# Kernel optimization log

Hardware: AMD Instinct MI355X
Metric: run time of the kernel (lower is better)

The kernel has to match this reference:

```python
import jax, jax.numpy as jnp
import numpy as np

B, S, D = 2, 2048, 2048
H = 16
HD = D // H  # 128

def setup_inputs() -> dict:
    key = jax.random.key(0)
    k1, k2, k3 = jax.random.split(key, 3)
    x = jax.random.normal(k1, (B, S, D), dtype=jnp.float32)
    w_qkv = jax.random.normal(k2, (D, 3 * D), dtype=jnp.float32) * (1.0 / np.sqrt(D))
    b_qkv = jnp.zeros((3 * D,), dtype=jnp.float32)
    w_out = jax.random.normal(k3, (D, D), dtype=jnp.float32) * (1.0 / np.sqrt(D))
    b_out = jnp.zeros((D,), dtype=jnp.float32)
    return {"x": x, "w_qkv": w_qkv, "b_qkv": b_qkv, "w_out": w_out, "b_out": b_out}

def reference(x, w_qkv, b_qkv, w_out, b_out):
    batch, seq_len, channels = x.shape
    qkv = x @ w_qkv + b_qkv                      # [B,S,3D]
    q, k, v = jnp.split(qkv, 3, axis=-1)
    # [B,S,D] -> [B,H,S,HD]
    def heads(t):
        return t.reshape(batch, seq_len, H, HD).transpose(0, 2, 1, 3)
    q, k, v = heads(q), heads(k), heads(v)
    scale = 1.0 / np.sqrt(HD).astype(np.float32)
    attn = jnp.einsum('bhqd,bhkd->bhqk', q, k) * scale
    causal = jnp.tril(jnp.ones((seq_len, seq_len), dtype=bool))
    attn = jnp.where(causal, attn, -jnp.inf)
    attn = jax.nn.softmax(attn, axis=-1)
    y = jnp.einsum('bhqk,bhkd->bhqd', attn, v)   # [B,H,S,HD]
    y = y.transpose(0, 2, 1, 3).reshape(batch, seq_len, channels)
    return y @ w_out + b_out
```

## Files before the change

kernel.cpp:

```cpp
#include <hip/hip_runtime.h>
#include <hip/hip_bf16.h>
#include <cstdint>
#include <cstddef>

#define BB 2
#define SS 2048
#define DD 2048
#define HH 16
#define HDIM 128
#define QSCALE 0.12751743f

typedef short bf16x8 __attribute__((ext_vector_type(8)));
typedef float f32x4 __attribute__((ext_vector_type(4)));
typedef float f32x16 __attribute__((ext_vector_type(16)));

__device__ __forceinline__ ushort f2bf(float f) {
    union { float f; uint32_t u; } v; v.f = f;
    uint32_t u = v.u;
    u += 0x7fffu + ((u >> 16) & 1u);
    return (ushort)(u >> 16);
}

__device__ __forceinline__ ushort f2bf_fast(float f) {
    union { float f; uint32_t u; } v; v.f = f;
    return (ushort)((v.u + 0x8000u) >> 16);
}

__device__ __forceinline__ void gl16(const ushort* g, ushort* l) {
    __builtin_amdgcn_global_load_lds(
        (const __attribute__((address_space(1))) unsigned int*)g,
        (__attribute__((address_space(3))) unsigned int*)l,
        16, 0, 0);
}


__global__ __launch_bounds__(256) void cast_x_kernel(
    const float* __restrict__ X, ushort* __restrict__ Xb)
{
    size_t idx = ((size_t)blockIdx.x * 256 + threadIdx.x) * 8;
    float4 a = *(const float4*)(X + idx);
    float4 b = *(const float4*)(X + idx + 4);
    ushort4 o0, o1;
    o0.x = f2bf(a.x); o0.y = f2bf(a.y); o0.z = f2bf(a.z); o0.w = f2bf(a.w);
    o1.x = f2bf(b.x); o1.y = f2bf(b.y); o1.z = f2bf(b.z); o1.w = f2bf(b.w);
    *(ushort4*)(Xb + idx) = o0;
    *(ushort4*)(Xb + idx + 4) = o1;
}

__global__ __launch_bounds__(256) void transpose_cast_kernel(
    const float* __restrict__ W, ushort* __restrict__ Wt, int K, int N)
{
    __shared__ ushort tile[32][36];
    const int n0 = blockIdx.x * 32;
    const int k0 = blockIdx.y * 32;
    const int t = threadIdx.x;
    const int r = t >> 3;
    const int c = (t & 7) * 4;
    float4 a = *(const float4*)(W + (size_t)(k0 + r) * N + n0 + c);
    tile[r][c + 0] = f2bf(a.x); tile[r][c + 1] = f2bf(a.y);
    tile[r][c + 2] = f2bf(a.z); tile[r][c + 3] = f2bf(a.w);
    __syncthreads();
    ushort4 o;
    o.x = tile[c + 0][r]; o.y = tile[c + 1][r];
    o.z = tile[c + 2][r]; o.w = tile[c + 3][r];
    *(ushort4*)(Wt + (size_t)(n0 + r) * K + k0 + c) = o;
}

__global__ __launch_bounds__(256) void transpose_v_kernel(
    const ushort* __restrict__ V, ushort* __restrict__ Vt)
{
    __shared__ ushort tile[32][36];
    const int s0 = blockIdx.x * 32;
    const int h0 = blockIdx.y * 32;
    const int bh = blockIdx.z;
    const ushort* Vp = V + (size_t)bh * SS * HDIM;
    ushort* Vtp = Vt + (size_t)bh * HDIM * SS;
    const int t = threadIdx.x;
    const int r = t >> 3;
    const int c = (t & 7) * 4;
    *(ushort4*)&tile[r][c] = *(const ushort4*)(Vp + (size_t)(s0 + r) * HDIM + h0 + c);
    __syncthreads();
    ushort4 o;
    o.x = tile[c + 0][r]; o.y = tile[c + 1][r];
    o.z = tile[c + 2][r]; o.w = tile[c + 3][r];
    *(ushort4*)(Vtp + (size_t)(h0 + r) * SS + s0 + c) = o;
}

__global__ __launch_bounds__(256) void gemm_qkv_kernel(
    const ushort* __restrict__ A, const ushort* __restrict__ Bt,
    const float* __restrict__ bias,
    ushort* __restrict__ Qo, ushort* __restrict__ Ko, ushort* __restrict__ Vo)
{
    const int n0 = blockIdx.x * 128;
    const int m0 = blockIdx.y * 128;
    __shared__ ushort As[128 * 32];
    __shared__ ushort Bs[128 * 32];
    const int t = threadIdx.x, w = t >> 6, lane = t & 63;
    const int l31 = lane & 31, hh = lane >> 5;
    const int lrow = lane >> 2, lks = lane & 3;
    const int wr = w >> 1, wc = w & 1;
    const int swst = (lrow >> 1) & 3;
    const int swr  = (l31 >> 1) & 3;

    f32x16 acc[2][2];
#pragma unroll
    for (int i = 0; i < 2; ++i)
#pragma unroll
        for (int j = 0; j < 2; ++j) acc[i][j] = (f32x16)0.f;

    for (int k0 = 0; k0 < DD; k0 += 32) {
        __syncthreads();
#pragma unroll
        for (int q = 0; q < 2; ++q) {
            int e = w * 2 + q;
            int row = e * 16 + lrow;
            gl16(A  + (size_t)(m0 + row) * DD + k0 + (lks ^ swst) * 8, &As[e * 512]);
            gl16(Bt + (size_t)(n0 + row) * DD + k0 + (lks ^ swst) * 8, &Bs[e * 512]);
        }
        __syncthreads();
#pragma unroll
        for (int k16 = 0; k16 < 2; ++k16) {
            int co = ((k16 * 2 + hh) ^ swr) * 8;
            bf16x8 ar0 = *(const bf16x8*)&As[(wr * 64 + l31) * 32 + co];
            bf16x8 ar1 = *(const bf16x8*)&As[(wr * 64 + 32 + l31) * 32 + co];
            bf16x8 br0 = *(const bf16x8*)&Bs[(wc * 64 + l31) * 32 + co];
            bf16x8 br1 = *(const bf16x8*)&Bs[(wc * 64 + 32 + l31) * 32 + co];
            acc[0][0] = __builtin_amdgcn_mfma_f32_32x32x16_bf16(ar0, br0, acc[0][0], 0, 0, 0);
            acc[0][1] = __builtin_amdgcn_mfma_f32_32x32x16_bf16(ar0, br1, acc[0][1], 0, 0, 0);
            acc[1][0] = __builtin_amdgcn_mfma_f32_32x32x16_bf16(ar1, br0, acc[1][0], 0, 0, 0);
            acc[1][1] = __builtin_amdgcn_mfma_f32_32x32x16_bf16(ar1, br1, acc[1][1], 0, 0, 0);
        }
    }

    const int bidx = m0 >> 11;
    const int which = n0 >> 11;
    ushort* dst = (which == 0) ? Qo : ((which == 1) ? Ko : Vo);
    const float sc = (which == 0) ? QSCALE : 1.0f;
#pragma unroll
    for (int j = 0; j < 2; ++j) {
        int n = n0 + wc * 64 + j * 32 + l31;
        int c = n & 2047, h = c >> 7, hd = c & 127;
        float bv = bias[n];
        size_t base = ((size_t)(bidx * HH + h) * SS) * HDIM + hd;
#pragma unroll
        for (int i = 0; i < 2; ++i) {
#pragma unroll
            for (int r = 0; r < 16; ++r) {
                int s = (m0 & 2047) + wr * 64 + i * 32 + (r & 3) + 8 * (r >> 2) + 4 * hh;
                dst[base + (size_t)s * HDIM] = f2bf((acc[i][j][r] + bv) * sc);
            }
        }
    }
}

__global__ __launch_bounds__(256) void gemm_out_kernel(
    const ushort* __restrict__ A, const ushort* __restrict__ Bt,
    const float* __restrict__ bias, float* __restrict__ Out)
{
    const int n0 = blockIdx.x * 128;
    const int m0 = blockIdx.y * 128;
    __shared__ ushort As[128 * 32];
    __shared__ ushort Bs[128 * 32];
    const int t = threadIdx.x, w = t >> 6, lane = t & 63;
    const int l31 = lane & 31, hh = lane >> 5;
    const int lrow = lane >> 2, lks = lane & 3;
    const int wr = w >> 1, wc = w & 1;
    const int swst = (lrow >> 1) & 3;
    const int swr  = (l31 >> 1) & 3;

    f32x16 acc[2][2];
#pragma unroll
    for (int i = 0; i < 2; ++i)
#pragma unroll
        for (int j = 0; j < 2; ++j) acc[i][j] = (f32x16)0.f;

    for (int k0 = 0; k0 < DD; k0 += 32) {
        __syncthreads();
#pragma unroll
        for (int q = 0; q < 2; ++q) {
            int e = w * 2 + q;
            int row = e * 16 + lrow;
            gl16(A  + (size_t)(m0 + row) * DD + k0 + (lks ^ swst) * 8, &As[e * 512]);
            gl16(Bt + (size_t)(n0 + row) * DD + k0 + (lks ^ swst) * 8, &Bs[e * 512]);
        }
        __syncthreads();
#pragma unroll
        for (int k16 = 0; k16 < 2; ++k16) {
            int co = ((k16 * 2 + hh) ^ swr) * 8;
            bf16x8 ar0 = *(const bf16x8*)&As[(wr * 64 + l31) * 32 + co];
            bf16x8 ar1 = *(const bf16x8*)&As[(wr * 64 + 32 + l31) * 32 + co];
            bf16x8 br0 = *(const bf16x8*)&Bs[(wc * 64 + l31) * 32 + co];
            bf16x8 br1 = *(const bf16x8*)&Bs[(wc * 64 + 32 + l31) * 32 + co];
            acc[0][0] = __builtin_amdgcn_mfma_f32_32x32x16_bf16(ar0, br0, acc[0][0], 0, 0, 0);
            acc[0][1] = __builtin_amdgcn_mfma_f32_32x32x16_bf16(ar0, br1, acc[0][1], 0, 0, 0);
            acc[1][0] = __builtin_amdgcn_mfma_f32_32x32x16_bf16(ar1, br0, acc[1][0], 0, 0, 0);
            acc[1][1] = __builtin_amdgcn_mfma_f32_32x32x16_bf16(ar1, br1, acc[1][1], 0, 0, 0);
        }
    }

#pragma unroll
    for (int j = 0; j < 2; ++j) {
        int n = n0 + wc * 64 + j * 32 + l31;
        float bv = bias[n];
#pragma unroll
        for (int i = 0; i < 2; ++i) {
#pragma unroll
            for (int r = 0; r < 16; ++r) {
                int m = m0 + wr * 64 + i * 32 + (r & 3) + 8 * (r >> 2) + 4 * hh;
                Out[(size_t)m * DD + n] = acc[i][j][r] + bv;
            }
        }
    }
}

__global__ __launch_bounds__(256, 2) void attn_mfma_kernel(
    const ushort* __restrict__ Q, const ushort* __restrict__ K,
    const ushort* __restrict__ Vt, ushort* __restrict__ Y)
{
    const int bh = blockIdx.y;
    const int qt = gridDim.x - 1 - blockIdx.x;
    const int q0 = qt * 128;
    const int b = bh >> 4, h = bh & 15;

    __shared__ ushort Ks[4 * 64 * 32];
    __shared__ ushort Vs[2 * 128 * 32];
    __shared__ ushort Ps[128 * 32];

    const int t = threadIdx.x, w = t >> 6, lane = t & 63;
    const int l31 = lane & 31, hh = lane >> 5;
    const int lrow = lane >> 2, lks = lane & 3;
    const int swst = (lrow >> 1) & 3;
    const int swr  = (l31 >> 1) & 3;

    const ushort* Qp = Q  + (size_t)bh * SS * HDIM;
    const ushort* Kp = K  + (size_t)bh * SS * HDIM;
    const ushort* Vp = Vt + (size_t)bh * HDIM * SS;

    bf16x8 aq[8];
#pragma unroll
    for (int kb2 = 0; kb2 < 8; ++kb2)
        aq[kb2] = *(const bf16x8*)(Qp + (size_t)(q0 + w * 32 + l31) * HDIM + kb2 * 16 + hh * 8);

    bf16x8 ones;
#pragma unroll
    for (int j = 0; j < 8; ++j) ones[j] = (short)0x3F80;

    f32x16 O[4];
#pragma unroll
    for (int nt = 0; nt < 4; ++nt) O[nt] = (f32x16)0.f;
    f32x16 Ol = (f32x16)0.f;

    const int kbdiag = 2 * qt + (w >> 1);
    const int nkb = 2 * qt + 2;

    for (int kb = 0; kb < nkb; ++kb) {
        const int kbase = kb * 64;
        __syncthreads();
#pragma unroll
        for (int g = 0; g < 4; ++g) {
            int key = g * 16 + lrow;
            gl16(Kp + (size_t)(kbase + key) * HDIM + w * 32 + (lks ^ swst) * 8,
                 &Ks[w * 2048 + g * 512]);
        }
#pragma unroll
        for (int g = 0; g < 4; ++g) {
            int pan = g >> 1, sub = g & 1;
            int dim = w * 32 + sub * 16 + lrow;
            gl16(Vp + (size_t)dim * SS + kbase + pan * 32 + (lks ^ swst) * 8,
                 &Vs[pan * 4096 + (w * 32 + sub * 16) * 32]);
        }
        __syncthreads();

        const bool active = (kb <= kbdiag);
        if (active) {
            f32x16 sc0 = (f32x16)0.f, sc1 = (f32x16)0.f;
#pragma unroll
            for (int kb2 = 0; kb2 < 8; ++kb2) {
                int co = (((kb2 & 1) * 2 + hh) ^ swr) * 8;
                bf16x8 bk0 = *(const bf16x8*)&Ks[(kb2 >> 1) * 2048 + l31 * 32 + co];
                bf16x8 bk1 = *(const bf16x8*)&Ks[(kb2 >> 1) * 2048 + (32 + l31) * 32 + co];
                sc0 = __builtin_amdgcn_mfma_f32_32x32x16_bf16(aq[kb2], bk0, sc0, 0, 0, 0);
                sc1 = __builtin_amdgcn_mfma_f32_32x32x16_bf16(aq[kb2], bk1, sc1, 0, 0, 0);
            }

            if (kb == kbdiag) {
#pragma unroll
                for (int r = 0; r < 16; ++r) {
                    int rowg = q0 + w * 32 + (r & 3) + 8 * (r >> 2) + 4 * hh;
                    if (kbase + l31 > rowg)      sc0[r] = -1e30f;
                    if (kbase + 32 + l31 > rowg) sc1[r] = -1e30f;
                }
            }

#pragma unroll
            for (int half = 0; half < 2; ++half) {
#pragma unroll
                for (int r = 0; r < 16; ++r) {
                    float sv = (half == 0) ? sc0[r] : sc1[r];
                    float p = __builtin_amdgcn_exp2f(sv);
                    int rowm = (r & 3) + 8 * (r >> 2) + 4 * hh;
                    int pc = (l31 >> 3) ^ ((rowm >> 1) & 3);
                    Ps[(w * 32 + rowm) * 32 + (pc << 3) + (l31 & 7)] = f2bf_fast(p);
                }
#pragma unroll
                for (int kblk2 = 0; kblk2 < 2; ++kblk2) {
                    int co = ((kblk2 * 2 + hh) ^ swr) * 8;
                    bf16x8 ap = *(const bf16x8*)&Ps[(w * 32 + l31) * 32 + co];
#pragma unroll
                    for (int nt = 0; nt < 4; ++nt) {
                        bf16x8 bv = *(const bf16x8*)&Vs[half * 4096 + (nt * 32 + l31) * 32 + co];
                        O[nt] = __builtin_amdgcn_mfma_f32_32x32x16_bf16(ap, bv, O[nt], 0, 0, 0);
                    }
                    Ol = __builtin_amdgcn_mfma_f32_32x32x16_bf16(ap, ones, Ol, 0, 0, 0);
                }
            }
        }
    }

#pragma unroll
    for (int r = 0; r < 16; ++r) {
        int s = q0 + w * 32 + (r & 3) + 8 * (r >> 2) + 4 * hh;
        float inv = 1.0f / Ol[r];
        size_t base = ((size_t)(b * SS + s)) * DD + h * HDIM;
#pragma unroll
        for (int nt = 0; nt < 4; ++nt)
            Y[base + nt * 32 + l31] = f2bf(O[nt][r] * inv);
    }
}

extern "C" void kernel_launch(void* const* d_in, const int* in_sizes, int n_in,
                              void* d_out, int out_size, void* d_ws, size_t ws_size,
                              hipStream_t stream) {
    const float* x     = (const float*)d_in[0];
    const float* w_qkv = (const float*)d_in[1];
    const float* b_qkv = (const float*)d_in[2];
    const float* w_out = (const float*)d_in[3];
    const float* b_out = (const float*)d_in[4];
    float* out = (float*)d_out;

    ushort* ws  = (ushort*)d_ws;
    ushort* xb  = ws;
    ushort* wtq = xb + 8388608;
    ushort* wto = wtq + 12582912;
    ushort* q   = wto + 4194304;
    ushort* k   = q + 8388608;
    ushort* v   = k + 8388608;
    ushort* vt  = v + 8388608;
    ushort* y   = vt + 8388608;

    cast_x_kernel<<<4096, 256, 0, stream>>>(x, xb);
    transpose_cast_kernel<<<dim3(192, 64), 256, 0, stream>>>(w_qkv, wtq, DD, 3 * DD);
    transpose_cast_kernel<<<dim3(64, 64), 256, 0, stream>>>(w_out, wto, DD, DD);
    gemm_qkv_kernel<<<dim3(48, 32), 256, 0, stream>>>(xb, wtq, b_qkv, q, k, v);
    transpose_v_kernel<<<dim3(64, 4, 32), 256, 0, stream>>>(v, vt);
    attn_mfma_kernel<<<dim3(16, 32), 256, 0, stream>>>(q, k, vt, y);
    gemm_out_kernel<<<dim3(16, 32), 256, 0, stream>>>(y, wto, b_out, out);
}
```

Baseline: 408.0 us.

## Rewrite QKV GEMM with 256x256 tiles, double-buffered LDS and ping-pong scheduling

Replaces the 128x128 single-buffered QKV projection GEMM with a 512-thread, 256x256-tile kernel. It uses a BK=64 double-buffered LDS pipeline, staggered global_load_lds prefetches interleaved with 16x16x32 MFMA phases, s_setprio, and an XCD-aware block remapping. The goal is to raise data reuse and hide global-load latency behind MFMA work, cutting memory-bound stalls in the largest GEMM. In exchange it uses much more LDS (128KB) and many more accumulator registers, so occupancy drops to one block per CU and correctness depends on hand-placed waitcnts.

```diff
diff --git a/kernel.cpp b/kernel.cpp
--- a/kernel.cpp
+++ b/kernel.cpp
@@ -32,7 +32,6 @@
         (__attribute__((address_space(3))) unsigned int*)l,
         16, 0, 0);
 }
-
 
 __global__ __launch_bounds__(256) void cast_x_kernel(
     const float* __restrict__ X, ushort* __restrict__ Xb)
@@ -86,10 +85,174 @@
     *(ushort4*)(Vtp + (size_t)(h0 + r) * SS + s0 + c) = o;
 }
 
-__global__ __launch_bounds__(256) void gemm_qkv_kernel(
+#define NTK 32
+
+__global__ __launch_bounds__(512) void gemm_qkv_kernel(
     const ushort* __restrict__ A, const ushort* __restrict__ Bt,
     const float* __restrict__ bias,
     ushort* __restrict__ Qo, ushort* __restrict__ Ko, ushort* __restrict__ Vo)
+{
+    const int bid = blockIdx.x;
+    const int wgid = (bid & 7) * 48 + (bid >> 3);
+    const int mt = wgid / 24;
+    const int nt = wgid - mt * 24;
+    const int m0 = mt * 256, n0 = nt * 256;
+
+    __shared__ ushort As[2][2][8192];
+    __shared__ ushort Bs[2][2][8192];
+
+    const int tid = threadIdx.x;
+    const int w = tid >> 6, lane = tid & 63;
+    const int wr = w >> 2, wc = w & 3;
+    const int l15 = lane & 15, l4x = lane >> 4, l7 = lane & 7;
+
+    const int rt  = w * 8 + (lane >> 3);
+    const int giA = (lane & 7) ^ (lane >> 3);
+    const size_t aoff = (size_t)(m0 + rt) * DD + giA * 8;
+    const int nb = (w >> 2) * 64 + (w & 3) * 8 + (lane >> 3);
+    const size_t boff = (size_t)(n0 + nb) * DD + giA * 8;
+    const int ldst = w * 512;
+
+    const int rdA = (wr * 64 + l15) << 7;
+    const int rdB = (wc * 32 + l15) << 7;
+    const int cb0 = (l4x ^ l7) << 4;
+    const int cb1 = ((l4x ^ l7) ^ 4) << 4;
+
+#define STAGE_A(t, qm) do { \
+    gl16(A + aoff + (size_t)((qm) * 64) * DD + (t) * 64,       &As[(t) & 1][qm][ldst]); \
+    gl16(A + aoff + (size_t)(128 + (qm) * 64) * DD + (t) * 64, &As[(t) & 1][qm][4096 + ldst]); \
+} while (0)
+#define STAGE_B(t, qn) do { \
+    gl16(Bt + boff + (size_t)((qn) * 32) * DD + (t) * 64,       &Bs[(t) & 1][qn][ldst]); \
+    gl16(Bt + boff + (size_t)(128 + (qn) * 32) * DD + (t) * 64, &Bs[(t) & 1][qn][4096 + ldst]); \
+} while (0)
+#define MFMA(d, x, y) d = __builtin_amdgcn_mfma_f32_16x16x32_bf16(x, y, d, 0, 0, 0)
+
+    f32x4 acc[8][4];
+#pragma unroll
+    for (int i = 0; i < 8; ++i)
+#pragma unroll
+        for (int j = 0; j < 4; ++j) acc[i][j] = (f32x4)0.f;
+
+    bf16x8 a[4][2], b0[2][2], b1[2][2];
+
+    STAGE_A(0, 0); STAGE_B(0, 1); STAGE_B(0, 0); STAGE_A(0, 1);
+    STAGE_A(1, 0); STAGE_B(1, 1);
+    asm volatile("s_waitcnt vmcnt(4)" ::: "memory");
+    __builtin_amdgcn_s_barrier();
+
+#pragma unroll 1
+    for (int t = 0; t < NTK; ++t) {
+        const char* Ab = (const char*)As + (t & 1) * 32768;
+        const char* Bb = (const char*)Bs + (t & 1) * 32768;
+
+#pragma unroll
+        for (int mf = 0; mf < 4; ++mf) {
+            a[mf][0] = *(const bf16x8*)(Ab + rdA + mf * 2048 + cb0);
+            a[mf][1] = *(const bf16x8*)(Ab + rdA + mf * 2048 + cb1);
+        }
+#pragma unroll
+        for (int nf = 0; nf < 2; ++nf) {
+            b0[nf][0] = *(const bf16x8*)(Bb + rdB + nf * 2048 + cb0);
+            b0[nf][1] = *(const bf16x8*)(Bb + rdB + nf * 2048 + cb1);
+        }
+        if (t + 1 < NTK) STAGE_B(t + 1, 0);
+        __builtin_amdgcn_s_barrier();
+        asm volatile("s_waitcnt lgkmcnt(0)" ::: "memory");
+        __builtin_amdgcn_s_setprio(1);
+#pragma unroll
+        for (int mf = 0; mf < 4; ++mf)
+#pragma unroll
+            for (int nf = 0; nf < 2; ++nf) {
+                MFMA(acc[mf][nf], a[mf][0], b0[nf][0]);
+                MFMA(acc[mf][nf], a[mf][1], b0[nf][1]);
+            }
+        __builtin_amdgcn_s_setprio(0);
+        __builtin_amdgcn_s_barrier();
+
+#pragma unroll
+        for (int nf = 0; nf < 2; ++nf) {
+            b1[nf][0] = *(const bf16x8*)(Bb + 16384 + rdB + nf * 2048 + cb0);
+            b1[nf][1] = *(const bf16x8*)(Bb + 16384 + rdB + nf * 2048 + cb1);
+        }
+        if (t + 1 < NTK) STAGE_A(t + 1, 1);
+        __builtin_amdgcn_s_barrier();
+        asm volatile("s_waitcnt lgkmcnt(0)" ::: "memory");
+        __builtin_amdgcn_s_setprio(1);
+#pragma unroll
+        for (int mf = 0; mf < 4; ++mf)
+#pragma unroll
+            for (int nf = 0; nf < 2; ++nf) {
+                MFMA(acc[mf][2 + nf], a[mf][0], b1[nf][0]);
+                MFMA(acc[mf][2 + nf], a[mf][1], b1[nf][1]);
+            }
+        __builtin_amdgcn_s_setprio(0);
+        __builtin_amdgcn_s_barrier();
+
+#pragma unroll
+        for (int mf = 0; mf < 4; ++mf) {
+            a[mf][0] = *(const bf16x8*)(Ab + 16384 + rdA + mf * 2048 + cb0);
+            a[mf][1] = *(const bf16x8*)(Ab + 16384 + rdA + mf * 2048 + cb1);
+        }
+        if (t + 2 < NTK) STAGE_A(t + 2, 0);
+        __builtin_amdgcn_s_barrier();
+        asm volatile("s_waitcnt lgkmcnt(0)" ::: "memory");
+        __builtin_amdgcn_s_setprio(1);
+#pragma unroll
+        for (int mf = 0; mf < 4; ++mf)
+#pragma unroll
+            for (int nf = 0; nf < 2; ++nf) {
+                MFMA(acc[4 + mf][2 + nf], a[mf][0], b1[nf][0]);
+                MFMA(acc[4 + mf][2 + nf], a[mf][1], b1[nf][1]);
+            }
+        __builtin_amdgcn_s_setprio(0);
+        __builtin_amdgcn_s_barrier();
+
+        if (t + 2 < NTK) STAGE_B(t + 2, 1);
+        __builtin_amdgcn_s_barrier();
+        __builtin_amdgcn_s_setprio(1);
+#pragma unroll
+        for (int mf = 0; mf < 4; ++mf)
+#pragma unroll
+            for (int nf = 0; nf < 2; ++nf) {
+                MFMA(acc[4 + mf][nf], a[mf][0], b0[nf][0]);
+                MFMA(acc[4 + mf][nf], a[mf][1], b0[nf][1]);
+            }
+        __builtin_amdgcn_s_setprio(0);
+        if (t + 2 < NTK)      { asm volatile("s_waitcnt vmcnt(4)" ::: "memory"); }
+        else if (t + 1 < NTK) { asm volatile("s_waitcnt vmcnt(0)" ::: "memory"); }
+        __builtin_amdgcn_s_barrier();
+    }
+#undef STAGE_A
+#undef STAGE_B
+#undef MFMA
+
+    const int which = n0 >> 11;
+    ushort* dst = (which == 0) ? Qo : ((which == 1) ? Ko : Vo);
+    const float sc = (which == 0) ? QSCALE : 1.0f;
+    const int bidx = m0 >> 11;
+    const int srow = (m0 & 2047) + wr * 128 + l4x * 4;
+#pragma unroll
+    for (int NF = 0; NF < 4; ++NF) {
+        int n = n0 + wc * 64 + NF * 16 + l15;
+        int cch = n & 2047;
+        int h = cch >> 7, hd = cch & 127;
+        float bv = bias[n];
+        size_t base = ((size_t)(bidx * HH + h) * SS) * HDIM + hd;
+#pragma unroll
+        for (int MF = 0; MF < 8; ++MF) {
+#pragma unroll
+            for (int r = 0; r < 4; ++r) {
+                int s = srow + MF * 16 + r;
+                dst[base + (size_t)s * HDIM] = f2bf((acc[MF][NF][r] + bv) * sc);
+            }
+        }
+    }
+}
+
+__global__ __launch_bounds__(256) void gemm_out_kernel(
+    const ushort* __restrict__ A, const ushort* __restrict__ Bt,
+    const float* __restrict__ bias, float* __restrict__ Out)
 {
     const int n0 = blockIdx.x * 128;
     const int m0 = blockIdx.y * 128;
@@ -132,72 +295,6 @@
         }
     }
 
-    const int bidx = m0 >> 11;
-    const int which = n0 >> 11;
-    ushort* dst = (which == 0) ? Qo : ((which == 1) ? Ko : Vo);
-    const float sc = (which == 0) ? QSCALE : 1.0f;
-#pragma unroll
-    for (int j = 0; j < 2; ++j) {
-        int n = n0 + wc * 64 + j * 32 + l31;
-        int c = n & 2047, h = c >> 7, hd = c & 127;
-        float bv = bias[n];
-        size_t base = ((size_t)(bidx * HH + h) * SS) * HDIM + hd;
-#pragma unroll
-        for (int i = 0; i < 2; ++i) {
-#pragma unroll
-            for (int r = 0; r < 16; ++r) {
-                int s = (m0 & 2047) + wr * 64 + i * 32 + (r & 3) + 8 * (r >> 2) + 4 * hh;
-                dst[base + (size_t)s * HDIM] = f2bf((acc[i][j][r] + bv) * sc);
-            }
-        }
-    }
-}
-
-__global__ __launch_bounds__(256) void gemm_out_kernel(
-    const ushort* __restrict__ A, const ushort* __restrict__ Bt,
-    const float* __restrict__ bias, float* __restrict__ Out)
-{
-    const int n0 = blockIdx.x * 128;
-    const int m0 = blockIdx.y * 128;
-    __shared__ ushort As[128 * 32];
-    __shared__ ushort Bs[128 * 32];
-    const int t = threadIdx.x, w = t >> 6, lane = t & 63;
-    const int l31 = lane & 31, hh = lane >> 5;
-    const int lrow = lane >> 2, lks = lane & 3;
-    const int wr = w >> 1, wc = w & 1;
-    const int swst = (lrow >> 1) & 3;
-    const int swr  = (l31 >> 1) & 3;
-
-    f32x16 acc[2][2];
-#pragma unroll
-    for (int i = 0; i < 2; ++i)
-#pragma unroll
-        for (int j = 0; j < 2; ++j) acc[i][j] = (f32x16)0.f;
-
-    for (int k0 = 0; k0 < DD; k0 += 32) {
-        __syncthreads();
-#pragma unroll
-        for (int q = 0; q < 2; ++q) {
-            int e = w * 2 + q;
-            int row = e * 16 + lrow;
-            gl16(A  + (size_t)(m0 + row) * DD + k0 + (lks ^ swst) * 8, &As[e * 512]);
-            gl16(Bt + (size_t)(n0 + row) * DD + k0 + (lks ^ swst) * 8, &Bs[e * 512]);
-        }
-        __syncthreads();
-#pragma unroll
-        for (int k16 = 0; k16 < 2; ++k16) {
-            int co = ((k16 * 2 + hh) ^ swr) * 8;
-            bf16x8 ar0 = *(const bf16x8*)&As[(wr * 64 + l31) * 32 + co];
-            bf16x8 ar1 = *(const bf16x8*)&As[(wr * 64 + 32 + l31) * 32 + co];
-            bf16x8 br0 = *(const bf16x8*)&Bs[(wc * 64 + l31) * 32 + co];
-            bf16x8 br1 = *(const bf16x8*)&Bs[(wc * 64 + 32 + l31) * 32 + co];
-            acc[0][0] = __builtin_amdgcn_mfma_f32_32x32x16_bf16(ar0, br0, acc[0][0], 0, 0, 0);
-            acc[0][1] = __builtin_amdgcn_mfma_f32_32x32x16_bf16(ar0, br1, acc[0][1], 0, 0, 0);
-            acc[1][0] = __builtin_amdgcn_mfma_f32_32x32x16_bf16(ar1, br0, acc[1][0], 0, 0, 0);
-            acc[1][1] = __builtin_amdgcn_mfma_f32_32x32x16_bf16(ar1, br1, acc[1][1], 0, 0, 0);
-        }
-    }
-
 #pragma unroll
     for (int j = 0; j < 2; ++j) {
         int n = n0 + wc * 64 + j * 32 + l31;
@@ -351,7 +448,7 @@
     cast_x_kernel<<<4096, 256, 0, stream>>>(x, xb);
     transpose_cast_kernel<<<dim3(192, 64), 256, 0, stream>>>(w_qkv, wtq, DD, 3 * DD);
     transpose_cast_kernel<<<dim3(64, 64), 256, 0, stream>>>(w_out, wto, DD, DD);
-    gemm_qkv_kernel<<<dim3(48, 32), 256, 0, stream>>>(xb, wtq, b_qkv, q, k, v);
+    gemm_qkv_kernel<<<384, 512, 0, stream>>>(xb, wtq, b_qkv, q, k, v);
     transpose_v_kernel<<<dim3(64, 4, 32), 256, 0, stream>>>(v, vt);
     attn_mfma_kernel<<<dim3(16, 32), 256, 0, stream>>>(q, k, vt, y);
     gemm_out_kernel<<<dim3(16, 32), 256, 0, stream>>>(y, wto, b_out, out);
```

New measurement: 400.4 us. No clear change (-1.9%).

## Double-buffer K/V tiles in attention kernel with async prefetch

Applied to the files above, without the earlier changes.

Turns the K and V shared-memory tiles into two slots and issues the global-to-LDS loads for the next key block before computing on the current one. Explicit vmcnt waits and raw barriers replace the two __syncthreads per iteration. It also raises wave priority around the MFMA sections. This doubles K/V LDS usage, which may cut occupancy at two blocks per CU, and relies on the vmcnt(8) count matching the eight loads issued per thread.

```diff
diff --git a/kernel.cpp b/kernel.cpp
--- a/kernel.cpp
+++ b/kernel.cpp
@@ -32,7 +32,6 @@
         (__attribute__((address_space(3))) unsigned int*)l,
         16, 0, 0);
 }
-
 
 __global__ __launch_bounds__(256) void cast_x_kernel(
     const float* __restrict__ X, ushort* __restrict__ Xb)
@@ -222,8 +221,8 @@
     const int q0 = qt * 128;
     const int b = bh >> 4, h = bh & 15;
 
-    __shared__ ushort Ks[4 * 64 * 32];
-    __shared__ ushort Vs[2 * 128 * 32];
+    __shared__ ushort Ks[2][4 * 64 * 32];
+    __shared__ ushort Vs[2][2 * 128 * 32];
     __shared__ ushort Ps[128 * 32];
 
     const int t = threadIdx.x, w = t >> 6, lane = t & 63;
@@ -253,35 +252,52 @@
     const int kbdiag = 2 * qt + (w >> 1);
     const int nkb = 2 * qt + 2;
 
+#define STAGE_KV(kb_, s_) do {                                                  \
+    const int kbase_ = (kb_) * 64;                                              \
+    _Pragma("unroll")                                                           \
+    for (int g = 0; g < 4; ++g) {                                               \
+        int key = g * 16 + lrow;                                                \
+        gl16(Kp + (size_t)(kbase_ + key) * HDIM + w * 32 + (lks ^ swst) * 8,    \
+             &Ks[s_][w * 2048 + g * 512]);                                      \
+    }                                                                           \
+    _Pragma("unroll")                                                           \
+    for (int g = 0; g < 4; ++g) {                                               \
+        int pan = g >> 1, sub = g & 1;                                          \
+        int dim = w * 32 + sub * 16 + lrow;                                     \
+        gl16(Vp + (size_t)dim * SS + kbase_ + pan * 32 + (lks ^ swst) * 8,      \
+             &Vs[s_][pan * 4096 + (w * 32 + sub * 16) * 32]);                   \
+    }                                                                           \
+} while (0)
+
+    STAGE_KV(0, 0);
+
     for (int kb = 0; kb < nkb; ++kb) {
         const int kbase = kb * 64;
-        __syncthreads();
-#pragma unroll
-        for (int g = 0; g < 4; ++g) {
-            int key = g * 16 + lrow;
-            gl16(Kp + (size_t)(kbase + key) * HDIM + w * 32 + (lks ^ swst) * 8,
-                 &Ks[w * 2048 + g * 512]);
-        }
-#pragma unroll
-        for (int g = 0; g < 4; ++g) {
-            int pan = g >> 1, sub = g & 1;
-            int dim = w * 32 + sub * 16 + lrow;
-            gl16(Vp + (size_t)dim * SS + kbase + pan * 32 + (lks ^ swst) * 8,
-                 &Vs[pan * 4096 + (w * 32 + sub * 16) * 32]);
-        }
-        __syncthreads();
-
-        const bool active = (kb <= kbdiag);
-        if (active) {
+        const int slot = kb & 1;
+
+        if (kb + 1 < nkb) {
+            STAGE_KV(kb + 1, slot ^ 1);
+            asm volatile("s_waitcnt vmcnt(8)" ::: "memory");
+        } else {
+            asm volatile("s_waitcnt vmcnt(0)" ::: "memory");
+        }
+        __builtin_amdgcn_s_barrier();
+
+        const ushort* KsS = Ks[slot];
+        const ushort* VsS = Vs[slot];
+
+        if (kb <= kbdiag) {
             f32x16 sc0 = (f32x16)0.f, sc1 = (f32x16)0.f;
+            __builtin_amdgcn_s_setprio(1);
 #pragma unroll
             for (int kb2 = 0; kb2 < 8; ++kb2) {
                 int co = (((kb2 & 1) * 2 + hh) ^ swr) * 8;
-                bf16x8 bk0 = *(const bf16x8*)&Ks[(kb2 >> 1) * 2048 + l31 * 32 + co];
-                bf16x8 bk1 = *(const bf16x8*)&Ks[(kb2 >> 1) * 2048 + (32 + l31) * 32 + co];
+                bf16x8 bk0 = *(const bf16x8*)&KsS[(kb2 >> 1) * 2048 + l31 * 32 + co];
+                bf16x8 bk1 = *(const bf16x8*)&KsS[(kb2 >> 1) * 2048 + (32 + l31) * 32 + co];
                 sc0 = __builtin_amdgcn_mfma_f32_32x32x16_bf16(aq[kb2], bk0, sc0, 0, 0, 0);
                 sc1 = __builtin_amdgcn_mfma_f32_32x32x16_bf16(aq[kb2], bk1, sc1, 0, 0, 0);
             }
+            __builtin_amdgcn_s_setprio(0);
 
             if (kb == kbdiag) {
 #pragma unroll
@@ -302,20 +318,24 @@
                     int pc = (l31 >> 3) ^ ((rowm >> 1) & 3);
                     Ps[(w * 32 + rowm) * 32 + (pc << 3) + (l31 & 7)] = f2bf_fast(p);
                 }
+                __builtin_amdgcn_s_setprio(1);
 #pragma unroll
                 for (int kblk2 = 0; kblk2 < 2; ++kblk2) {
                     int co = ((kblk2 * 2 + hh) ^ swr) * 8;
                     bf16x8 ap = *(const bf16x8*)&Ps[(w * 32 + l31) * 32 + co];
 #pragma unroll
                     for (int nt = 0; nt < 4; ++nt) {
-                        bf16x8 bv = *(const bf16x8*)&Vs[half * 4096 + (nt * 32 + l31) * 32 + co];
+                        bf16x8 bv = *(const bf16x8*)&VsS[half * 4096 + (nt * 32 + l31) * 32 + co];
                         O[nt] = __builtin_amdgcn_mfma_f32_32x32x16_bf16(ap, bv, O[nt], 0, 0, 0);
                     }
                     Ol = __builtin_amdgcn_mfma_f32_32x32x16_bf16(ap, ones, Ol, 0, 0, 0);
                 }
-            }
-        }
-    }
+                __builtin_amdgcn_s_setprio(0);
+            }
+        }
+        __builtin_amdgcn_s_barrier();
+    }
+#undef STAGE_KV
 
 #pragma unroll
     for (int r = 0; r < 16; ++r) {
```

After: 399.6 us. 1.02x faster.
